# Performance work log

Measured on AMD Instinct MI355X. Metric: run time of the kernel, lower is better.

## Reference

```python
import jax, jax.numpy as jnp
import numpy as np

B, S, N = 16, 128, 64            # batch, sentence length, padded KB-word slots per sentence
E, DK, H, L = 128, 128, 128, 32  # char embed, kb embed, per-direction hidden (hidden_size=2H), labels
CHAR_NUM, KB_NUM = 8000, 200000


def setup_inputs():
    key = jax.random.key(0)
    ks = jax.random.split(key, 40)
    u = lambda k, sh: jax.random.uniform(k, sh, jnp.float32, -0.08, 0.08)
    inp = {
        "char_ids": jax.random.randint(ks[0], (B, S), 0, CHAR_NUM),
        "kb_word_ids": jax.random.randint(ks[1], (B, N), 0, KB_NUM),
        "word_begin": jax.random.randint(ks[2], (B, N), 0, S),
        "word_len": jax.random.randint(ks[3], (B, N), 0, 6),
        "label": jax.random.randint(ks[4], (B, S), 0, L),
        "sequence_length": jax.random.randint(ks[5], (B,), S // 2, S + 1),
        "char_emb": u(ks[6], (CHAR_NUM, E)),
        "kb_emb": u(ks[7], (KB_NUM, DK)),
        "dense_W": u(ks[8], (2 * H, L)),
        "dense_b": jnp.zeros((L,), jnp.float32),
        "crf_T": u(ks[9], (L, L)),
    }
    i = 10
    for p in ("f", "r"):
        inp[p + "_Wcx"] = u(ks[i], (E, 4 * H))
        inp[p + "_Wch"] = u(ks[i + 1], (H, 4 * H))
        inp[p + "_bc"] = jnp.zeros((4 * H,), jnp.float32)
        inp[p + "_Wwx"] = u(ks[i + 2], (DK, 3 * H))
        inp[p + "_Wwh"] = u(ks[i + 3], (H, 3 * H))
        inp[p + "_bw"] = jnp.zeros((3 * H,), jnp.float32)
        inp[p + "_Wlx"] = u(ks[i + 4], (E, H))
        inp[p + "_Wlc"] = u(ks[i + 5], (H, H))
        inp[p + "_bl"] = jnp.zeros((H,), jnp.float32)
        i += 6
    return inp


def _lattice_dir(X, Xw, begin, end, pos_valid, word_valid,
                 Wcx, Wch, bc, Wwx, Wwh, bw, Wlx, Wlc, bl):
    # X:[S,E] chars in scan order, Xw:[N,DK] KB words, begin/end:[N] span indices
    # in scan order (end inclusive), pos_valid:[S] bool, word_valid:[N] bool.
    Xg = X @ Wcx + bc    # [S,4H] hoisted char-gate input projection
    Xl = X @ Wlx + bl    # [S,H]  hoisted link-gate input projection
    Wg = Xw @ Wwx + bw   # [N,3H] hoisted word-gate input projection

    def step(carry, t):
        h_hist, c_hist = carry                 # [S+1,H]; slot k = state after step k-1
        h_prev, c_prev = h_hist[t], c_hist[t]
        gi, gf, go, gg = jnp.split(Xg[t] + h_prev @ Wch, 4)
        i = jax.nn.sigmoid(gi); f = jax.nn.sigmoid(gf)
        o = jax.nn.sigmoid(go); g = jnp.tanh(gg)
        # word cells: built from the state just before each word's begin position
        hb, cb = h_hist[begin], c_hist[begin]  # [N,H]
        wi, wf, wg = jnp.split(Wg + hb @ Wwh, 3, axis=1)
        cw = jax.nn.sigmoid(wf) * cb + jax.nn.sigmoid(wi) * jnp.tanh(wg)  # [N,H]
        lg = jax.nn.sigmoid(Xl[t] + cw @ Wlc)  # [N,H] link gates
        wmask = ((end == t) & word_valid).astype(X.dtype)[:, None]
        ew = jnp.exp(lg) * wmask
        ec = jnp.exp(i)
        c_lat = (ec * g + (ew * cw).sum(0)) / (ec + ew.sum(0))  # gate-normalized merge
        c_std = f * c_prev + i * g             # plain LSTM step when no word ends at t
        c_t = jnp.where(wmask.sum() > 0, c_lat, c_std)
        h_t = o * jnp.tanh(c_t)
        v = pos_valid[t]
        h_hist = h_hist.at[t + 1].set(jnp.where(v, h_t, h_prev))
        c_hist = c_hist.at[t + 1].set(jnp.where(v, c_t, c_prev))
        return (h_hist, c_hist), jnp.where(v, h_t, jnp.zeros_like(h_t))

    init = (jnp.zeros((S + 1, H), X.dtype), jnp.zeros((S + 1, H), X.dtype))
    _, hs = jax.lax.scan(step, init, jnp.arange(S))
    return hs  # [S,H]


def _forward(char_ids, kb_word_ids, word_begin, word_len, label, sequence_length,
             char_emb, kb_emb, dense_W, dense_b, crf_T, fparams, rparams):
    X = char_emb[char_ids]            # [B,S,E]
    Xw = kb_emb[kb_word_ids]          # [B,N,DK]
    end = jnp.minimum(word_begin + word_len, S - 1)   # inclusive span end
    word_valid = end < sequence_length[:, None]       # whole span inside sentence
    pos = jnp.arange(S)
    pv_f = pos[None, :] < sequence_length[:, None]
    fwd = jax.vmap(lambda x, xw, b, e, pv, wv:
                   _lattice_dir(x, xw, b, e, pv, wv, *fparams))(
        X, Xw, word_begin, end, pv_f, word_valid)
    # backward direction: flip time axis; span (b,e) maps to (S-1-e, S-1-b)
    pv_r = pos[None, :] >= (S - sequence_length)[:, None]
    bwd = jax.vmap(lambda x, xw, b, e, pv, wv:
                   _lattice_dir(x, xw, b, e, pv, wv, *rparams))(
        X[:, ::-1], Xw, S - 1 - end, S - 1 - word_begin, pv_r, word_valid)[:, ::-1]
    feats = jnp.concatenate([fwd, bwd], axis=-1)      # [B,S,2H]
    logits = feats @ dense_W + dense_b                # [B,S,L]
    # CRF negative log-likelihood
    mask = pv_f.astype(logits.dtype)                  # [B,S]
    emit = jnp.take_along_axis(logits, label[..., None], axis=2)[..., 0]
    trans = crf_T[label[:, :-1], label[:, 1:]]
    gold = (emit * mask).sum(1) + (trans * mask[:, 1:]).sum(1)

    def fstep(alpha, xs):
        logit_t, m_t = xs
        new = jax.scipy.special.logsumexp(alpha[:, :, None] + crf_T[None], axis=1) + logit_t
        return jnp.where(m_t[:, None] > 0, new, alpha), None

    alpha, _ = jax.lax.scan(fstep, logits[:, 0],
                            (logits[:, 1:].transpose(1, 0, 2), mask[:, 1:].T))
    logZ = jax.scipy.special.logsumexp(alpha, axis=1)
    return jnp.mean(logZ - gold)


def reference(char_ids, kb_word_ids, word_begin, word_len, label, sequence_length,
              char_emb, kb_emb, dense_W, dense_b, crf_T,
              f_Wcx, f_Wch, f_bc, f_Wwx, f_Wwh, f_bw, f_Wlx, f_Wlc, f_bl,
              r_Wcx, r_Wch, r_bc, r_Wwx, r_Wwh, r_bw, r_Wlx, r_Wlc, r_bl):
    fparams = (f_Wcx, f_Wch, f_bc, f_Wwx, f_Wwh, f_bw, f_Wlx, f_Wlc, f_bl)
    rparams = (r_Wcx, r_Wch, r_bc, r_Wwx, r_Wwh, r_bw, r_Wlx, r_Wlc, r_bl)
    return _forward(char_ids, kb_word_ids, word_begin, word_len, label, sequence_length,
                    char_emb, kb_emb, dense_W, dense_b, crf_T, fparams, rparams)
```

## Files before the change

kernel.cpp:

```cpp
#include <hip/hip_runtime.h>


typedef _Float16 f16x2 __attribute__((ext_vector_type(2)));

__device__ __forceinline__ float sigm(float x) { return 1.f / (1.f + __expf(-x)); }
__device__ __forceinline__ float tanh_fast(float x) {
    return 1.f - 2.f / (__expf(2.f * x) + 1.f);
}
__device__ __forceinline__ void bar_lgkm() {
    asm volatile("s_waitcnt lgkmcnt(0)\n\ts_barrier" ::: "memory");
}

#if defined(__has_builtin)
#if __has_builtin(__builtin_amdgcn_fdot2)
#define FDOT2(a, b, c) __builtin_amdgcn_fdot2((a), (b), (c), false)
#endif
#endif
#ifndef FDOT2
__device__ __forceinline__ float fdot2_sw(f16x2 a, f16x2 b, float c) {
    return fmaf((float)a.x, (float)b.x, fmaf((float)a.y, (float)b.y, c));
}
#define FDOT2(a, b, c) fdot2_sw((a), (b), (c))
#endif

template <int K, int J, int RPB, int BLK>
__global__ __launch_bounds__(BLK)
void gemm_pair(const float* __restrict__ emb, const int* __restrict__ idx,
               const float* __restrict__ W0, const float* __restrict__ W1,
               const float* __restrict__ b0, const float* __restrict__ b1,
               float* __restrict__ out, int rowsTotal, int Sdim, int revmode)
{
    constexpr int NJ4 = J / 4;
    constexpr int RT  = BLK / NJ4;
    constexpr int RPT = RPB / RT;
    static_assert(BLK % NJ4 == 0 && RPB % RT == 0, "layout");
    const int y = blockIdx.y;
    const float* __restrict__ W    = y ? W1 : W0;
    const float* __restrict__ bias = y ? b1 : b0;
    float* __restrict__ outp = out + (size_t)y * rowsTotal * J;
    const int rev = (revmode && y) ? 1 : 0;

    __shared__ __align__(16) float xs[RPB * K];
    __shared__ const float* srcs[RPB];
    const int tid = threadIdx.x;
    const int r0 = blockIdx.x * RPB;
    if (tid < RPB) {
        const int row = r0 + tid;
        const float* s = nullptr;
        if (row < rowsTotal) {
            if (idx) {
                const int bb = row / Sdim, tt = row - bb * Sdim;
                const int ts = rev ? (Sdim - 1 - tt) : tt;
                s = emb + (size_t)idx[bb * Sdim + ts] * K;
            } else {
                s = emb + (size_t)row * K;
            }
        }
        srcs[tid] = s;
    }
    __syncthreads();
    constexpr int NQ = RPB * K / 4;
    for (int q = tid; q < NQ; q += BLK) {
        const int rr = q / (K / 4), qq = q - rr * (K / 4);
        const float4* s = (const float4*)srcs[rr];
        ((float4*)xs)[q] = s ? s[qq] : make_float4(0.f, 0.f, 0.f, 0.f);
    }
    __syncthreads();

    const int jq = tid % NJ4;
    const int rg = tid / NJ4;
    float4 acc[RPT];
#pragma unroll
    for (int r = 0; r < RPT; ++r) acc[r] = make_float4(0.f, 0.f, 0.f, 0.f);
    const float4* __restrict__ W4 = (const float4*)W;
#pragma unroll 4
    for (int k = 0; k < K; ++k) {
        const float4 wv = W4[(size_t)k * NJ4 + jq];
#pragma unroll
        for (int r = 0; r < RPT; ++r) {
            const float xv = xs[(rg * RPT + r) * K + k];
            acc[r].x = fmaf(xv, wv.x, acc[r].x);
            acc[r].y = fmaf(xv, wv.y, acc[r].y);
            acc[r].z = fmaf(xv, wv.z, acc[r].z);
            acc[r].w = fmaf(xv, wv.w, acc[r].w);
        }
    }
    const float4 bv = ((const float4*)bias)[jq];
#pragma unroll
    for (int r = 0; r < RPT; ++r) {
        const int row = r0 + rg * RPT + r;
        if (row < rowsTotal)
            ((float4*)outp)[(size_t)row * NJ4 + jq] =
                make_float4(acc[r].x + bv.x, acc[r].y + bv.y,
                            acc[r].z + bv.z, acc[r].w + bv.w);
    }
}

#define HH_BYTES (129 * 128 * 2)
#define CH_BYTES (129 * 128 * 4)
#define LAT_DYN_SMEM (HH_BYTES + CH_BYTES)

__global__ __launch_bounds__(512, 2)
void lattice_kernel(const float* __restrict__ Xg,
                    const float* __restrict__ Xl,
                    const float* __restrict__ Wgp,
                    const float* __restrict__ Wch_f, const float* __restrict__ Wch_r,
                    const float* __restrict__ Wwh_f, const float* __restrict__ Wwh_r,
                    const float* __restrict__ Wlc_f, const float* __restrict__ Wlc_r,
                    const int* __restrict__ word_begin, const int* __restrict__ word_len,
                    const int* __restrict__ seqlen,
                    float* __restrict__ feats)
{
    extern __shared__ __align__(16) char dyn_smem[];
    _Float16* hh = (_Float16*)dyn_smem;
    float*    ch = (float*)(dyn_smem + HH_BYTES);

    const int bdid = blockIdx.x;
    const int b = bdid >> 1, dir = bdid & 1;
    const int tid = threadIdx.x;
    const int kc = tid >> 7;
    const int jj = tid & 127;

    const float* Wch = dir ? Wch_r : Wch_f;
    const float* Wwh = dir ? Wwh_r : Wwh_f;
    const float* Wlc = dir ? Wlc_r : Wlc_f;

    f16x2 wch2[64];
    {
        const float* base = Wch + (size_t)(kc * 32) * 512 + jj;
#pragma unroll
        for (int g = 0; g < 4; ++g)
#pragma unroll
            for (int u2 = 0; u2 < 16; ++u2) {
                f16x2 v;
                v.x = (_Float16)base[(size_t)(2 * u2) * 512 + g * 128];
                v.y = (_Float16)base[(size_t)(2 * u2 + 1) * 512 + g * 128];
                wch2[g * 16 + u2] = v;
            }
    }
    f16x2 wwh2[48];
    {
        const float* base = Wwh + (size_t)(kc * 32) * 384 + jj;
#pragma unroll
        for (int g = 0; g < 3; ++g)
#pragma unroll
            for (int u2 = 0; u2 < 16; ++u2) {
                f16x2 v;
                v.x = (_Float16)base[(size_t)(2 * u2) * 384 + g * 128];
                v.y = (_Float16)base[(size_t)(2 * u2 + 1) * 384 + g * 128];
                wwh2[g * 16 + u2] = v;
            }
    }
    f16x2 wlc2[16];
    {
        const float* base = Wlc + (size_t)(kc * 32) * 128 + jj;
#pragma unroll
        for (int u2 = 0; u2 < 16; ++u2) {
            f16x2 v;
            v.x = (_Float16)base[(size_t)(2 * u2) * 128];
            v.y = (_Float16)base[(size_t)(2 * u2 + 1) * 128];
            wlc2[u2] = v;
        }
    }

    __shared__ __align__(16) float part[2048];
    __shared__ __align__(16) float wpart[2 * 1536];
    __shared__ __align__(16) float lpart[2 * 512];
    __shared__ __align__(16) _Float16 cw2s[2 * 128];
    __shared__ int ev_start[129];
    __shared__ int cnts[128];
    __shared__ int fills[128];
    __shared__ short ev_word[64];
    __shared__ short wbeg_s[64];

    const int sl = seqlen[b];

    if (tid < 128) { cnts[tid] = 0; fills[tid] = 0; }
    __syncthreads();
    int myvalid = 0, myed = 0;
    if (tid < 64) {
        const int bg = word_begin[b * 64 + tid];
        const int ln = word_len[b * 64 + tid];
        int ef = bg + ln; if (ef > 127) ef = 127;
        myvalid = (ef < sl);
        const int bd_ = dir ? (127 - ef) : bg;
        const int ed_ = dir ? (127 - bg) : ef;
        wbeg_s[tid] = (short)bd_;
        myed = ed_;
        if (myvalid) atomicAdd(&cnts[ed_], 1);
    }
    __syncthreads();
    if (tid == 0) {
        int run = 0; ev_start[0] = 0;
        for (int t = 0; t < 128; ++t) { run += cnts[t]; ev_start[t + 1] = run; }
    }
    __syncthreads();
    if (tid < 64 && myvalid) {
        const int pos = atomicAdd(&fills[myed], 1);
        ev_word[ev_start[myed] + pos] = (short)tid;
    }
    if (tid < 128) { hh[tid] = (_Float16)0.f; ch[tid] = 0.f; }
    __syncthreads();

    const float* Xg_b = Xg + ((size_t)dir * 2048 + (size_t)b * 128) * 512;
    const float* Xl_b = Xl + ((size_t)dir * 2048 + (size_t)b * 128) * 128;
    const float* Wg_b = Wgp + ((size_t)dir * 1024 + (size_t)b * 64) * 384;

    float h_reg = 0.f, c_reg = 0.f;
    float xg_cur = Xg_b[tid];

    for (int t = 0; t < 128; ++t) {
        const int e0 = ev_start[t];
        const int E  = ev_start[t + 1] - e0;
        const int ec0 = E < 2 ? E : 2;

        int bgs[2] = {0, 0};
        float wgp[2][3];
        float xl = 0.f;
#pragma unroll
        for (int s = 0; s < 2; ++s)
            if (s < ec0) {
                const int w = ev_word[e0 + s];
                bgs[s] = wbeg_s[w];
                if (tid < 128) {
                    const float* wgr = Wg_b + (size_t)w * 384;
                    wgp[s][0] = wgr[tid]; wgp[s][1] = wgr[128 + tid]; wgp[s][2] = wgr[256 + tid];
                }
            }
        if (E > 0 && tid < 128) xl = Xl_b[(size_t)t * 128 + tid];
        const float xg_nxt = (t < 127) ? Xg_b[(size_t)(t + 1) * 512 + tid] : 0.f;

        {
            const f16x2* hrow = (const f16x2*)(hh + (size_t)t * 128) + kc * 16;
            f16x2 hv[16];
#pragma unroll
            for (int u2 = 0; u2 < 16; ++u2) hv[u2] = hrow[u2];
            float p0 = 0.f, p1 = 0.f, p2 = 0.f, p3 = 0.f;
#pragma unroll
            for (int u2 = 0; u2 < 16; ++u2) {
                p0 = FDOT2(wch2[u2],      hv[u2], p0);
                p1 = FDOT2(wch2[16 + u2], hv[u2], p1);
                p2 = FDOT2(wch2[32 + u2], hv[u2], p2);
                p3 = FDOT2(wch2[48 + u2], hv[u2], p3);
            }
            if      (kc == 0) p0 += xg_cur;
            else if (kc == 1) p1 += xg_cur;
            else if (kc == 2) p2 += xg_cur;
            else              p3 += xg_cur;
            part[kc * 512 +       jj] = p0;
            part[kc * 512 + 128 + jj] = p1;
            part[kc * 512 + 256 + jj] = p2;
            part[kc * 512 + 384 + jj] = p3;
        }
#pragma unroll
        for (int s = 0; s < 2; ++s)
            if (s < ec0) {
                const f16x2* hbrow = (const f16x2*)(hh + (size_t)bgs[s] * 128) + kc * 16;
                float q0 = 0.f, q1 = 0.f, q2 = 0.f;
#pragma unroll
                for (int u2 = 0; u2 < 16; ++u2) {
                    const f16x2 hb = hbrow[u2];
                    q0 = FDOT2(wwh2[u2],      hb, q0);
                    q1 = FDOT2(wwh2[16 + u2], hb, q1);
                    q2 = FDOT2(wwh2[32 + u2], hb, q2);
                }
                wpart[s * 1536 + kc * 384 +       jj] = q0;
                wpart[s * 1536 + kc * 384 + 128 + jj] = q1;
                wpart[s * 1536 + kc * 384 + 256 + jj] = q2;
            }
        bar_lgkm();

        float gi = 0.f, gf = 0.f, go = 0.f, gg = 0.f;
        float cwreg[2] = {0.f, 0.f};
        if (tid < 128) {
            const float a0 = part[tid]       + part[512 + tid]  + part[1024 + tid] + part[1536 + tid];
            const float a1 = part[128 + tid] + part[640 + tid]  + part[1152 + tid] + part[1664 + tid];
            const float a2 = part[256 + tid] + part[768 + tid]  + part[1280 + tid] + part[1792 + tid];
            const float a3 = part[384 + tid] + part[896 + tid]  + part[1408 + tid] + part[1920 + tid];
            gi = sigm(a0); gf = sigm(a1); go = sigm(a2); gg = tanh_fast(a3);
#pragma unroll
            for (int s = 0; s < 2; ++s)
                if (s < ec0) {
                    const int sb = s * 1536;
                    const float cb = ch[(size_t)bgs[s] * 128 + tid];
                    const float wi = wgp[s][0] + wpart[sb + tid]       + wpart[sb + 384 + tid] + wpart[sb + 768 + tid]  + wpart[sb + 1152 + tid];
                    const float wf = wgp[s][1] + wpart[sb + 128 + tid] + wpart[sb + 512 + tid] + wpart[sb + 896 + tid]  + wpart[sb + 1280 + tid];
                    const float wv = wgp[s][2] + wpart[sb + 256 + tid] + wpart[sb + 640 + tid] + wpart[sb + 1024 + tid] + wpart[sb + 1408 + tid];
                    const float cwv = sigm(wf) * cb + sigm(wi) * tanh_fast(wv);
                    cwreg[s] = cwv;
                    cw2s[s * 128 + tid] = (_Float16)cwv;
                }
        }

        float accn = 0.f, accd = 0.f;
        if (E > 0) {
            bar_lgkm();
            const int nc = (E + 1) >> 1;
            for (int c = 0; c < nc; ++c) {
                const int base = c * 2;
                const int en = (E - base) < 2 ? (E - base) : 2;
#pragma unroll
                for (int s = 0; s < 2; ++s)
                    if (s < en) {
                        const f16x2* cwrow = (const f16x2*)(cw2s + s * 128) + kc * 16;
                        float r = 0.f;
#pragma unroll
                        for (int u2 = 0; u2 < 16; ++u2) r = FDOT2(wlc2[u2], cwrow[u2], r);
                        lpart[s * 512 + kc * 128 + jj] = r;
                    }
                const int nb = base + 2;
                int nn = E - nb; nn = nn < 0 ? 0 : (nn > 2 ? 2 : nn);
                int bgs2[2] = {0, 0};
                float wgp2[2][3];
#pragma unroll
                for (int s = 0; s < 2; ++s)
                    if (s < nn) {
                        const int w = ev_word[e0 + nb + s];
                        bgs2[s] = wbeg_s[w];
                        if (tid < 128) {
                            const float* wgr = Wg_b + (size_t)w * 384;
                            wgp2[s][0] = wgr[tid]; wgp2[s][1] = wgr[128 + tid]; wgp2[s][2] = wgr[256 + tid];
                        }
                    }
#pragma unroll
                for (int s = 0; s < 2; ++s)
                    if (s < nn) {
                        const f16x2* hbrow = (const f16x2*)(hh + (size_t)bgs2[s] * 128) + kc * 16;
                        float q0 = 0.f, q1 = 0.f, q2 = 0.f;
#pragma unroll
                        for (int u2 = 0; u2 < 16; ++u2) {
                            const f16x2 hb = hbrow[u2];
                            q0 = FDOT2(wwh2[u2],      hb, q0);
                            q1 = FDOT2(wwh2[16 + u2], hb, q1);
                            q2 = FDOT2(wwh2[32 + u2], hb, q2);
                        }
                        wpart[s * 1536 + kc * 384 +       jj] = q0;
                        wpart[s * 1536 + kc * 384 + 128 + jj] = q1;
                        wpart[s * 1536 + kc * 384 + 256 + jj] = q2;
                    }
                bar_lgkm();
                if (tid < 128) {
#pragma unroll
                    for (int s = 0; s < 2; ++s)
                        if (s < en) {
                            const float lg = sigm(xl + lpart[s * 512 + tid] + lpart[s * 512 + 128 + tid]
                                                     + lpart[s * 512 + 256 + tid] + lpart[s * 512 + 384 + tid]);
                            const float ew = __expf(lg);
                            accn = fmaf(ew, cwreg[s], accn);
                            accd += ew;
                        }
#pragma unroll
                    for (int s = 0; s < 2; ++s)
                        if (s < nn) {
                            const int sb = s * 1536;
                            const float cb = ch[(size_t)bgs2[s] * 128 + tid];
                            const float wi = wgp2[s][0] + wpart[sb + tid]       + wpart[sb + 384 + tid] + wpart[sb + 768 + tid]  + wpart[sb + 1152 + tid];
                            const float wf = wgp2[s][1] + wpart[sb + 128 + tid] + wpart[sb + 512 + tid] + wpart[sb + 896 + tid]  + wpart[sb + 1280 + tid];
                            const float wv = wgp2[s][2] + wpart[sb + 256 + tid] + wpart[sb + 640 + tid] + wpart[sb + 1024 + tid] + wpart[sb + 1408 + tid];
                            const float cwv = sigm(wf) * cb + sigm(wi) * tanh_fast(wv);
                            cwreg[s] = cwv;
                            cw2s[s * 128 + tid] = (_Float16)cwv;
                        }
                }
                if (c + 1 < nc) bar_lgkm();
            }
        }

        if (tid < 128) {
            float c_t;
            if (E > 0) {
                const float ec = __expf(gi);
                c_t = (ec * gg + accn) / (ec + accd);
            } else {
                c_t = gf * c_reg + gi * gg;
            }
            const float h_t = go * tanh_fast(c_t);
            const bool v = dir ? (t >= 128 - sl) : (t < sl);
            const float hn = v ? h_t : h_reg;
            const float cn = v ? c_t : c_reg;
            h_reg = hn; c_reg = cn;
            hh[(size_t)(t + 1) * 128 + tid] = (_Float16)hn;
            ch[(size_t)(t + 1) * 128 + tid] = cn;
        }
        xg_cur = xg_nxt;
        bar_lgkm();
    }

    for (int i = tid; i < 128 * 128; i += 512) {
        const int t = i >> 7, j = i & 127;
        const bool v = dir ? (t >= 128 - sl) : (t < sl);
        const float hv = v ? (float)hh[(size_t)(t + 1) * 128 + j] : 0.f;
        const int s = dir ? (127 - t) : t;
        feats[((size_t)b * 128 + s) * 256 + dir * 128 + j] = hv;
    }
}

__global__ void crf_kernel(const float* __restrict__ logits,
                           const int* __restrict__ label,
                           const int* __restrict__ seqlen,
                           const float* __restrict__ T,
                           float* __restrict__ out_part)
{
    const int half = threadIdx.x >> 5;
    const int j    = threadIdx.x & 31;
    const int b    = blockIdx.x * 2 + half;

    float Tc[32];
#pragma unroll
    for (int i = 0; i < 32; ++i) Tc[i] = T[i * 32 + j];

    const float* lg = logits + (size_t)b * 128 * 32;
    const int* lab = label + b * 128;
    const int sl = seqlen[b];

    float g = 0.f;
#pragma unroll
    for (int r = 0; r < 4; ++r) {
        const int t = j + r * 32;
        if (t < sl) {
            g += lg[t * 32 + lab[t]];
            if (t >= 1) g += T[lab[t - 1] * 32 + lab[t]];
        }
    }
#pragma unroll
    for (int m = 16; m; m >>= 1) g += __shfl_xor(g, m, 32);

    __shared__ __align__(16) float alpha_s[2][32];
    float av = lg[j];
    alpha_s[half][j] = av;
    __syncthreads();
    for (int t = 1; t < 128; ++t) {
        float a[32];
        const float4* ap = (const float4*)alpha_s[half];
#pragma unroll
        for (int q = 0; q < 8; ++q) {
            const float4 v = ap[q];
            a[4 * q] = v.x; a[4 * q + 1] = v.y; a[4 * q + 2] = v.z; a[4 * q + 3] = v.w;
        }
        float m = -1e30f;
#pragma unroll
        for (int i = 0; i < 32; ++i) m = fmaxf(m, a[i] + Tc[i]);
        float s = 0.f;
#pragma unroll
        for (int i = 0; i < 32; ++i) s += __expf(a[i] + Tc[i] - m);
        float nv = m + __logf(s) + lg[t * 32 + j];
        if (t >= sl) nv = av;
        av = nv;
        __syncthreads();
        alpha_s[half][j] = av;
        __syncthreads();
    }
    float m2 = av;
#pragma unroll
    for (int m = 16; m; m >>= 1) m2 = fmaxf(m2, __shfl_xor(m2, m, 32));
    float s2 = __expf(av - m2);
#pragma unroll
    for (int m = 16; m; m >>= 1) s2 += __shfl_xor(s2, m, 32);
    if (j == 0) out_part[b] = (m2 + __logf(s2)) - g;
}

__global__ void finalize_kernel(const float* __restrict__ partb, float* __restrict__ out)
{
    if (threadIdx.x == 0 && blockIdx.x == 0) {
        float s = 0.f;
        for (int i = 0; i < 16; i++) s += partb[i];
        out[0] = s * (1.f / 16.f);
    }
}

extern "C" void kernel_launch(void* const* d_in, const int* in_sizes, int n_in,
                              void* d_out, int out_size, void* d_ws, size_t ws_size,
                              hipStream_t stream)
{
    (void)in_sizes; (void)n_in; (void)out_size; (void)ws_size;
    const int*   char_ids    = (const int*)d_in[0];
    const int*   kb_word_ids = (const int*)d_in[1];
    const int*   word_begin  = (const int*)d_in[2];
    const int*   word_len    = (const int*)d_in[3];
    const int*   label       = (const int*)d_in[4];
    const int*   seqlen      = (const int*)d_in[5];
    const float* char_emb    = (const float*)d_in[6];
    const float* kb_emb      = (const float*)d_in[7];
    const float* dense_W     = (const float*)d_in[8];
    const float* dense_b     = (const float*)d_in[9];
    const float* crf_T       = (const float*)d_in[10];
    const float* f_Wcx = (const float*)d_in[11];
    const float* f_Wch = (const float*)d_in[12];
    const float* f_bc  = (const float*)d_in[13];
    const float* f_Wwx = (const float*)d_in[14];
    const float* f_Wwh = (const float*)d_in[15];
    const float* f_bw  = (const float*)d_in[16];
    const float* f_Wlx = (const float*)d_in[17];
    const float* f_Wlc = (const float*)d_in[18];
    const float* f_bl  = (const float*)d_in[19];
    const float* r_Wcx = (const float*)d_in[20];
    const float* r_Wch = (const float*)d_in[21];
    const float* r_bc  = (const float*)d_in[22];
    const float* r_Wwx = (const float*)d_in[23];
    const float* r_Wwh = (const float*)d_in[24];
    const float* r_bw  = (const float*)d_in[25];
    const float* r_Wlx = (const float*)d_in[26];
    const float* r_Wlc = (const float*)d_in[27];
    const float* r_bl  = (const float*)d_in[28];

    float* ws = (float*)d_ws;
    size_t o = 0;
    float* Xg     = ws + o; o += (size_t)2 * 2048 * 512;
    float* Xl     = ws + o; o += (size_t)2 * 2048 * 128;
    float* Wg     = ws + o; o += (size_t)2 * 1024 * 384;
    float* feats  = ws + o; o += (size_t)2048 * 256;
    float* logits = ws + o; o += (size_t)2048 * 32;
    float* partb  = ws + o; o += 16;

    gemm_pair<128, 512, 8, 256><<<dim3(256, 2), 256, 0, stream>>>(
        char_emb, char_ids, f_Wcx, r_Wcx, f_bc, r_bc, Xg, 2048, 128, 1);
    gemm_pair<128, 128, 8, 256><<<dim3(256, 2), 256, 0, stream>>>(
        char_emb, char_ids, f_Wlx, r_Wlx, f_bl, r_bl, Xl, 2048, 128, 1);
    gemm_pair<128, 384, 8, 192><<<dim3(128, 2), 192, 0, stream>>>(
        kb_emb, kb_word_ids, f_Wwx, r_Wwx, f_bw, r_bw, Wg, 1024, 64, 0);

    lattice_kernel<<<32, 512, LAT_DYN_SMEM, stream>>>(
        Xg, Xl, Wg, f_Wch, r_Wch, f_Wwh, r_Wwh, f_Wlc, r_Wlc,
        word_begin, word_len, seqlen, feats);

    gemm_pair<256, 32, 16, 128><<<dim3(128, 1), 128, 0, stream>>>(
        feats, nullptr, dense_W, dense_W, dense_b, dense_b, logits, 2048, 128, 0);
    crf_kernel<<<8, 64, 0, stream>>>(logits, label, seqlen, crf_T, partb);
    finalize_kernel<<<1, 64, 0, stream>>>(partb, (float*)d_out);
}
```

Baseline: 539.3 us.

## Replace LDS partial-sum reductions with quad DPP reductions in lattice kernel

Thread mapping changes so the four K-chunks of each output column sit in adjacent lanes (kc = tid&3). Cross-chunk sums then use DPP quad shuffles instead of writing partials to shared memory and reading them back after a barrier. This removes several barriers per timestep and makes all 512 threads compute gates redundantly. Next-step word and Xl/Xg loads are also prefetched one step ahead, and the cell-word buffer is double-buffered. The cost is redundant activation math in all four lanes and more registers live across the loop.

```diff
diff --git a/kernel.cpp b/kernel.cpp
--- a/kernel.cpp
+++ b/kernel.cpp
@@ -22,6 +22,23 @@
 }
 #define FDOT2(a, b, c) fdot2_sw((a), (b), (c))
 #endif
+
+#if defined(__has_builtin)
+#if __has_builtin(__builtin_amdgcn_mov_dpp)
+#define HAVE_DPP 1
+#endif
+#endif
+
+__device__ __forceinline__ float quad_sum(float v) {
+#ifdef HAVE_DPP
+    v += __int_as_float(__builtin_amdgcn_mov_dpp(__float_as_int(v), 0xB1, 0xF, 0xF, true));
+    v += __int_as_float(__builtin_amdgcn_mov_dpp(__float_as_int(v), 0x4E, 0xF, 0xF, true));
+#else
+    v += __shfl_xor(v, 1);
+    v += __shfl_xor(v, 2);
+#endif
+    return v;
+}
 
 template <int K, int J, int RPB, int BLK>
 __global__ __launch_bounds__(BLK)
@@ -118,8 +135,8 @@
     const int bdid = blockIdx.x;
     const int b = bdid >> 1, dir = bdid & 1;
     const int tid = threadIdx.x;
-    const int kc = tid >> 7;
-    const int jj = tid & 127;
+    const int kc  = tid & 3;
+    const int jj  = tid >> 2;
 
     const float* Wch = dir ? Wch_r : Wch_f;
     const float* Wwh = dir ? Wwh_r : Wwh_f;
@@ -163,10 +180,7 @@
         }
     }
 
-    __shared__ __align__(16) float part[2048];
-    __shared__ __align__(16) float wpart[2 * 1536];
-    __shared__ __align__(16) float lpart[2 * 512];
-    __shared__ __align__(16) _Float16 cw2s[2 * 128];
+    __shared__ _Float16 cw2s[2][2][128];
     __shared__ int ev_start[129];
     __shared__ int cnts[128];
     __shared__ int fills[128];
@@ -207,35 +221,60 @@
     const float* Wg_b = Wgp + ((size_t)dir * 1024 + (size_t)b * 64) * 384;
 
     float h_reg = 0.f, c_reg = 0.f;
-    float xg_cur = Xg_b[tid];
+    const int xgoff = kc * 128 + jj;
+
+    int   curE, cur_ec0;
+    int   cur_bgs[2] = {0, 0};
+    float cur_wgp[2][3] = {};
+    float cur_xl = 0.f;
+    float xg_cur;
+    {
+        const int e0 = ev_start[0];
+        curE = ev_start[1] - e0;
+        cur_ec0 = curE < 2 ? curE : 2;
+#pragma unroll
+        for (int s = 0; s < 2; ++s)
+            if (s < cur_ec0) {
+                const int w = ev_word[e0 + s];
+                cur_bgs[s] = wbeg_s[w];
+                const float* wgr = Wg_b + (size_t)w * 384;
+                cur_wgp[s][0] = wgr[jj];
+                cur_wgp[s][1] = wgr[128 + jj];
+                cur_wgp[s][2] = wgr[256 + jj];
+            }
+        if (curE > 0) cur_xl = Xl_b[jj];
+        xg_cur = Xg_b[xgoff];
+    }
 
     for (int t = 0; t < 128; ++t) {
-        const int e0 = ev_start[t];
-        const int E  = ev_start[t + 1] - e0;
-        const int ec0 = E < 2 ? E : 2;
-
-        int bgs[2] = {0, 0};
-        float wgp[2][3];
-        float xl = 0.f;
-#pragma unroll
-        for (int s = 0; s < 2; ++s)
-            if (s < ec0) {
-                const int w = ev_word[e0 + s];
-                bgs[s] = wbeg_s[w];
-                if (tid < 128) {
+        int   nxtE = 0, nxt_ec0 = 0;
+        int   nxt_bgs[2] = {0, 0};
+        float nxt_wgp[2][3] = {};
+        float nxt_xl = 0.f, xg_nxt = 0.f;
+        if (t < 127) {
+            const int e0n = ev_start[t + 1];
+            nxtE = ev_start[t + 2] - e0n;
+            nxt_ec0 = nxtE < 2 ? nxtE : 2;
+#pragma unroll
+            for (int s = 0; s < 2; ++s)
+                if (s < nxt_ec0) {
+                    const int w = ev_word[e0n + s];
+                    nxt_bgs[s] = wbeg_s[w];
                     const float* wgr = Wg_b + (size_t)w * 384;
-                    wgp[s][0] = wgr[tid]; wgp[s][1] = wgr[128 + tid]; wgp[s][2] = wgr[256 + tid];
+                    nxt_wgp[s][0] = wgr[jj];
+                    nxt_wgp[s][1] = wgr[128 + jj];
+                    nxt_wgp[s][2] = wgr[256 + jj];
                 }
-            }
-        if (E > 0 && tid < 128) xl = Xl_b[(size_t)t * 128 + tid];
-        const float xg_nxt = (t < 127) ? Xg_b[(size_t)(t + 1) * 512 + tid] : 0.f;
-
+            if (nxtE > 0) nxt_xl = Xl_b[(size_t)(t + 1) * 128 + jj];
+            xg_nxt = Xg_b[(size_t)(t + 1) * 512 + xgoff];
+        }
+
+        float p0 = 0.f, p1 = 0.f, p2 = 0.f, p3 = 0.f;
         {
             const f16x2* hrow = (const f16x2*)(hh + (size_t)t * 128) + kc * 16;
             f16x2 hv[16];
 #pragma unroll
             for (int u2 = 0; u2 < 16; ++u2) hv[u2] = hrow[u2];
-            float p0 = 0.f, p1 = 0.f, p2 = 0.f, p3 = 0.f;
 #pragma unroll
             for (int u2 = 0; u2 < 16; ++u2) {
                 p0 = FDOT2(wch2[u2],      hv[u2], p0);
@@ -243,89 +282,74 @@
                 p2 = FDOT2(wch2[32 + u2], hv[u2], p2);
                 p3 = FDOT2(wch2[48 + u2], hv[u2], p3);
             }
-            if      (kc == 0) p0 += xg_cur;
-            else if (kc == 1) p1 += xg_cur;
-            else if (kc == 2) p2 += xg_cur;
-            else              p3 += xg_cur;
-            part[kc * 512 +       jj] = p0;
-            part[kc * 512 + 128 + jj] = p1;
-            part[kc * 512 + 256 + jj] = p2;
-            part[kc * 512 + 384 + jj] = p3;
-        }
+        }
+        float q[2][3];
+#pragma unroll
+        for (int s = 0; s < 2; ++s) { q[s][0] = 0.f; q[s][1] = 0.f; q[s][2] = 0.f; }
 #pragma unroll
         for (int s = 0; s < 2; ++s)
-            if (s < ec0) {
-                const f16x2* hbrow = (const f16x2*)(hh + (size_t)bgs[s] * 128) + kc * 16;
-                float q0 = 0.f, q1 = 0.f, q2 = 0.f;
+            if (s < cur_ec0) {
+                const f16x2* hbrow = (const f16x2*)(hh + (size_t)cur_bgs[s] * 128) + kc * 16;
 #pragma unroll
                 for (int u2 = 0; u2 < 16; ++u2) {
                     const f16x2 hb = hbrow[u2];
-                    q0 = FDOT2(wwh2[u2],      hb, q0);
-                    q1 = FDOT2(wwh2[16 + u2], hb, q1);
-                    q2 = FDOT2(wwh2[32 + u2], hb, q2);
+                    q[s][0] = FDOT2(wwh2[u2],      hb, q[s][0]);
+                    q[s][1] = FDOT2(wwh2[16 + u2], hb, q[s][1]);
+                    q[s][2] = FDOT2(wwh2[32 + u2], hb, q[s][2]);
                 }
-                wpart[s * 1536 + kc * 384 +       jj] = q0;
-                wpart[s * 1536 + kc * 384 + 128 + jj] = q1;
-                wpart[s * 1536 + kc * 384 + 256 + jj] = q2;
-            }
-        bar_lgkm();
-
-        float gi = 0.f, gf = 0.f, go = 0.f, gg = 0.f;
-        float cwreg[2] = {0.f, 0.f};
-        if (tid < 128) {
-            const float a0 = part[tid]       + part[512 + tid]  + part[1024 + tid] + part[1536 + tid];
-            const float a1 = part[128 + tid] + part[640 + tid]  + part[1152 + tid] + part[1664 + tid];
-            const float a2 = part[256 + tid] + part[768 + tid]  + part[1280 + tid] + part[1792 + tid];
-            const float a3 = part[384 + tid] + part[896 + tid]  + part[1408 + tid] + part[1920 + tid];
-            gi = sigm(a0); gf = sigm(a1); go = sigm(a2); gg = tanh_fast(a3);
+            }
+
+        if      (kc == 0) p0 += xg_cur;
+        else if (kc == 1) p1 += xg_cur;
+        else if (kc == 2) p2 += xg_cur;
+        else              p3 += xg_cur;
+
+        const float gi = sigm(quad_sum(p0));
+        const float gf = sigm(quad_sum(p1));
+        const float go = sigm(quad_sum(p2));
+        const float gg = tanh_fast(quad_sum(p3));
+
+        float accn = 0.f, accd = 0.f;
+        if (curE > 0) {
+            const int e0 = ev_start[t];
+            float cwcur[2] = {0.f, 0.f};
 #pragma unroll
             for (int s = 0; s < 2; ++s)
-                if (s < ec0) {
-                    const int sb = s * 1536;
-                    const float cb = ch[(size_t)bgs[s] * 128 + tid];
-                    const float wi = wgp[s][0] + wpart[sb + tid]       + wpart[sb + 384 + tid] + wpart[sb + 768 + tid]  + wpart[sb + 1152 + tid];
-                    const float wf = wgp[s][1] + wpart[sb + 128 + tid] + wpart[sb + 512 + tid] + wpart[sb + 896 + tid]  + wpart[sb + 1280 + tid];
-                    const float wv = wgp[s][2] + wpart[sb + 256 + tid] + wpart[sb + 640 + tid] + wpart[sb + 1024 + tid] + wpart[sb + 1408 + tid];
+                if (s < cur_ec0) {
+                    const float wi = cur_wgp[s][0] + quad_sum(q[s][0]);
+                    const float wf = cur_wgp[s][1] + quad_sum(q[s][1]);
+                    const float wv = cur_wgp[s][2] + quad_sum(q[s][2]);
+                    const float cb = ch[(size_t)cur_bgs[s] * 128 + jj];
                     const float cwv = sigm(wf) * cb + sigm(wi) * tanh_fast(wv);
-                    cwreg[s] = cwv;
-                    cw2s[s * 128 + tid] = (_Float16)cwv;
+                    cwcur[s] = cwv;
+                    if (kc == 0) cw2s[0][s][jj] = (_Float16)cwv;
                 }
-        }
-
-        float accn = 0.f, accd = 0.f;
-        if (E > 0) {
             bar_lgkm();
-            const int nc = (E + 1) >> 1;
+            const int nc = (curE + 1) >> 1;
             for (int c = 0; c < nc; ++c) {
-                const int base = c * 2;
-                const int en = (E - base) < 2 ? (E - base) : 2;
+                const int base2 = c * 2;
+                const int en = (curE - base2) < 2 ? (curE - base2) : 2;
+                float lgs[2] = {0.f, 0.f};
 #pragma unroll
                 for (int s = 0; s < 2; ++s)
                     if (s < en) {
-                        const f16x2* cwrow = (const f16x2*)(cw2s + s * 128) + kc * 16;
+                        const f16x2* cwrow = (const f16x2*)(&cw2s[c & 1][s][0]) + kc * 16;
                         float r = 0.f;
 #pragma unroll
                         for (int u2 = 0; u2 < 16; ++u2) r = FDOT2(wlc2[u2], cwrow[u2], r);
-                        lpart[s * 512 + kc * 128 + jj] = r;
+                        lgs[s] = quad_sum(r);
                     }
-                const int nb = base + 2;
-                int nn = E - nb; nn = nn < 0 ? 0 : (nn > 2 ? 2 : nn);
-                int bgs2[2] = {0, 0};
-                float wgp2[2][3];
+                const int nb = base2 + 2;
+                int nn = curE - nb; nn = nn < 0 ? 0 : (nn > 2 ? 2 : nn);
+                float cwnxt[2] = {0.f, 0.f};
 #pragma unroll
                 for (int s = 0; s < 2; ++s)
                     if (s < nn) {
                         const int w = ev_word[e0 + nb + s];
-                        bgs2[s] = wbeg_s[w];
-                        if (tid < 128) {
-                            const float* wgr = Wg_b + (size_t)w * 384;
-                            wgp2[s][0] = wgr[tid]; wgp2[s][1] = wgr[128 + tid]; wgp2[s][2] = wgr[256 + tid];
-                        }
-                    }
-#pragma unroll
-                for (int s = 0; s < 2; ++s)
-                    if (s < nn) {
-                        const f16x2* hbrow = (const f16x2*)(hh + (size_t)bgs2[s] * 128) + kc * 16;
+                        const int bg2 = wbeg_s[w];
+                        const float* wgr = Wg_b + (size_t)w * 384;
+                        const float wg0 = wgr[jj], wg1 = wgr[128 + jj], wg2 = wgr[256 + jj];
+                        const f16x2* hbrow = (const f16x2*)(hh + (size_t)bg2 * 128) + kc * 16;
                         float q0 = 0.f, q1 = 0.f, q2 = 0.f;
 #pragma unroll
                         for (int u2 = 0; u2 < 16; ++u2) {
@@ -334,54 +358,55 @@
                             q1 = FDOT2(wwh2[16 + u2], hb, q1);
                             q2 = FDOT2(wwh2[32 + u2], hb, q2);
                         }
-                        wpart[s * 1536 + kc * 384 +       jj] = q0;
-                        wpart[s * 1536 + kc * 384 + 128 + jj] = q1;
-                        wpart[s * 1536 + kc * 384 + 256 + jj] = q2;
+                        const float wi = wg0 + quad_sum(q0);
+                        const float wf = wg1 + quad_sum(q1);
+                        const float wv = wg2 + quad_sum(q2);
+                        const float cb = ch[(size_t)bg2 * 128 + jj];
+                        const float cwv = sigm(wf) * cb + sigm(wi) * tanh_fast(wv);
+                        cwnxt[s] = cwv;
+                        if (kc == 0) cw2s[(c + 1) & 1][s][jj] = (_Float16)cwv;
                     }
-                bar_lgkm();
-                if (tid < 128) {
-#pragma unroll
-                    for (int s = 0; s < 2; ++s)
-                        if (s < en) {
-                            const float lg = sigm(xl + lpart[s * 512 + tid] + lpart[s * 512 + 128 + tid]
-                                                     + lpart[s * 512 + 256 + tid] + lpart[s * 512 + 384 + tid]);
-                            const float ew = __expf(lg);
-                            accn = fmaf(ew, cwreg[s], accn);
-                            accd += ew;
-                        }
-#pragma unroll
-                    for (int s = 0; s < 2; ++s)
-                        if (s < nn) {
-                            const int sb = s * 1536;
-                            const float cb = ch[(size_t)bgs2[s] * 128 + tid];
-                            const float wi = wgp2[s][0] + wpart[sb + tid]       + wpart[sb + 384 + tid] + wpart[sb + 768 + tid]  + wpart[sb + 1152 + tid];
-                            const float wf = wgp2[s][1] + wpart[sb + 128 + tid] + wpart[sb + 512 + tid] + wpart[sb + 896 + tid]  + wpart[sb + 1280 + tid];
-                            const float wv = wgp2[s][2] + wpart[sb + 256 + tid] + wpart[sb + 640 + tid] + wpart[sb + 1024 + tid] + wpart[sb + 1408 + tid];
-                            const float cwv = sigm(wf) * cb + sigm(wi) * tanh_fast(wv);
-                            cwreg[s] = cwv;
-                            cw2s[s * 128 + tid] = (_Float16)cwv;
-                        }
+#pragma unroll
+                for (int s = 0; s < 2; ++s)
+                    if (s < en) {
+                        const float lg = sigm(cur_xl + lgs[s]);
+                        const float ew = __expf(lg);
+                        accn = fmaf(ew, cwcur[s], accn);
+                        accd += ew;
+                    }
+                if (c + 1 < nc) {
+                    bar_lgkm();
+                    cwcur[0] = cwnxt[0]; cwcur[1] = cwnxt[1];
                 }
-                if (c + 1 < nc) bar_lgkm();
-            }
-        }
-
-        if (tid < 128) {
-            float c_t;
-            if (E > 0) {
-                const float ec = __expf(gi);
-                c_t = (ec * gg + accn) / (ec + accd);
-            } else {
-                c_t = gf * c_reg + gi * gg;
-            }
-            const float h_t = go * tanh_fast(c_t);
-            const bool v = dir ? (t >= 128 - sl) : (t < sl);
-            const float hn = v ? h_t : h_reg;
-            const float cn = v ? c_t : c_reg;
-            h_reg = hn; c_reg = cn;
-            hh[(size_t)(t + 1) * 128 + tid] = (_Float16)hn;
-            ch[(size_t)(t + 1) * 128 + tid] = cn;
-        }
+            }
+        }
+
+        float c_t;
+        if (curE > 0) {
+            const float ec = __expf(gi);
+            c_t = (ec * gg + accn) / (ec + accd);
+        } else {
+            c_t = gf * c_reg + gi * gg;
+        }
+        const float h_t = go * tanh_fast(c_t);
+        const bool v = dir ? (t >= 128 - sl) : (t < sl);
+        const float hn = v ? h_t : h_reg;
+        const float cn = v ? c_t : c_reg;
+        h_reg = hn; c_reg = cn;
+        if (kc == 0) {
+            hh[(size_t)(t + 1) * 128 + jj] = (_Float16)hn;
+            ch[(size_t)(t + 1) * 128 + jj] = cn;
+        }
+
+        curE = nxtE; cur_ec0 = nxt_ec0;
+        cur_bgs[0] = nxt_bgs[0]; cur_bgs[1] = nxt_bgs[1];
+#pragma unroll
+        for (int s = 0; s < 2; ++s) {
+            cur_wgp[s][0] = nxt_wgp[s][0];
+            cur_wgp[s][1] = nxt_wgp[s][1];
+            cur_wgp[s][2] = nxt_wgp[s][2];
+        }
+        cur_xl = nxt_xl;
         xg_cur = xg_nxt;
         bar_lgkm();
     }
```

Result: faster. 523.2 us (-3.0%).
